# Optimization experiments

Hardware: AMD Instinct MI355X
Metric: run time of the kernel (lower is better)

Reference implementation:

```python
import jax, jax.numpy as jnp
import numpy as np

# AllOrNothing: spike threshold (x > 0) with straight-through gradient.
@jax.custom_vjp
def aon(x):
    return (x > 0).astype(x.dtype)

def _aon_fwd(x):
    return aon(x), None

def _aon_bwd(_, g):
    return (g,)

aon.defvjp(_aon_fwd, _aon_bwd)

T, B = 1000, 128
N_IN, N_H, N_PC, N_HD, N_IC = 3, 256, 256, 12, 268


def setup_inputs() -> dict:
    key = jax.random.key(0)
    ks = jax.random.split(key, 13)
    f32 = jnp.float32
    inp = {
        "x": jax.random.normal(ks[0], (T, B, N_IN), f32),
        "initial_conds": jax.random.normal(ks[1], (B, N_IC), f32),
        # RecurrentSNUCell params
        "iw": jax.random.normal(ks[2], (N_IN, N_H), f32) / np.sqrt(N_IN),  # kaiming-ish
        "l": jax.random.normal(ks[3], (N_H,), f32) / np.sqrt(N_H),          # trunc-normal-ish
        "b": jnp.zeros((N_H,), f32),
        # Linear layers, stored as [in, out] for x @ W + b
        "state_embed_w": jax.random.normal(ks[4], (N_IC, N_H), f32) / np.sqrt(128.0),
        "state_embed_b": jnp.zeros((N_H,), f32),
        "cell_embed_w": jax.random.normal(ks[5], (N_IC, N_H), f32) / np.sqrt(128.0),
        "cell_embed_b": jnp.zeros((N_H,), f32),
        "pc_w": jax.random.normal(ks[6], (N_H, N_PC), f32) / np.sqrt(256.0),
        "pc_b": jnp.zeros((N_PC,), f32),
        "hd_w": jax.random.normal(ks[7], (N_H, N_HD), f32) / np.sqrt(12.0),
        "hd_b": jnp.zeros((N_HD,), f32),
    }
    return inp


def reference(x, initial_conds, iw, l, b,
              state_embed_w, state_embed_b, cell_embed_w, cell_embed_b,
              pc_w, pc_b, hd_w, hd_b):
    # init = cat(initial_conds); here a single [B, 268] tensor
    h0 = jax.nn.sigmoid(initial_conds @ state_embed_w + state_embed_b)  # y_0 [B,H]
    c0 = jax.nn.sigmoid(initial_conds @ cell_embed_w + cell_embed_b)    # s_0 [B,H]

    def step(carry, x_t):
        h, c = carry  # (y_t, s_t)
        # RecurrentSNUCell: s = relu(x@iw + y + l*s*(1-y)); y = aon(s + b)
        s = jax.nn.relu(x_t @ iw + h + l * c * (1.0 - h))
        y = aon(s + b)
        # dropout in eval mode -> identity
        pc = y @ pc_w + pc_b
        hd = y @ hd_w + hd_b
        return (y, s), (hd, pc, y, y, s)

    _, (logits_hd, logits_pc, bottleneck_acts, rnn_states, cell_states) = \
        jax.lax.scan(step, (h0, c0), x)
    return (logits_hd, logits_pc, bottleneck_acts, rnn_states, cell_states)
```

## Files before the change

### kernel.cpp

```cpp
#include <hip/hip_runtime.h>
#include <hip/hip_bf16.h>
#include <math.h>

#define T_STEPS 1000
#define BATCH   128
#define NH      256
#define NIC     268
#define NHD     12

#define SZ_HD (T_STEPS * BATCH * NHD)
#define SZ_PC (T_STEPS * BATCH * NH)
#define OFF_HD 0
#define OFF_PC (SZ_HD)
#define OFF_BA (OFF_PC + SZ_PC)
#define OFF_RS (OFF_BA + SZ_PC)
#define OFF_CS (OFF_RS + SZ_PC)

typedef __attribute__((ext_vector_type(8))) short short8;
typedef __attribute__((ext_vector_type(4))) float float4v;

static __device__ __forceinline__ unsigned short f32_to_bf16_bits(float v) {
    __hip_bfloat16 h = __float2bfloat16(v);
    return *reinterpret_cast<unsigned short*>(&h);
}

__global__ __launch_bounds__(64) void recurrence_kernel(
    const float* __restrict__ x,
    const float* __restrict__ ic,
    const float* __restrict__ iw,
    const float* __restrict__ l,
    const float* __restrict__ bvec,
    const float* __restrict__ sew,
    const float* __restrict__ seb,
    const float* __restrict__ cew,
    const float* __restrict__ ceb,
    float* __restrict__ out)
{
    const int blk = blockIdx.x;
    const int b   = blk >> 2;
    const int h   = ((blk & 3) << 6) | (threadIdx.x & 63);

    double ah = (double)seb[h];
    double ac = (double)ceb[h];
    const float* icrow = ic + (size_t)b * NIC;
    for (int k = 0; k < NIC; ++k) {
        const double v = (double)icrow[k];
        ah += v * (double)sew[(size_t)k * NH + h];
        ac += v * (double)cew[(size_t)k * NH + h];
    }
    double y = 1.0 / (1.0 + exp(-ah));
    double c = 1.0 / (1.0 + exp(-ac));

    const double lv = (double)l[h];
    const double bv = (double)bvec[h];
    const double w0 = (double)iw[h];
    const double w1 = (double)iw[NH + h];
    const double w2 = (double)iw[2 * NH + h];

    const float* xp = x + (size_t)b * 3;
    float* __restrict__ out_ba = out + OFF_BA;
    float* __restrict__ out_rs = out + OFF_RS;
    float* __restrict__ out_cs = out + OFF_CS;

    const size_t obase = (size_t)b * NH + h;

    float bufA[30], bufB[30];

    auto pre_load = [&](float* bf, int tb) {
#pragma unroll
        for (int u = 0; u < 10; ++u) {
            const float* p = xp + (size_t)(tb + u) * (BATCH * 3);
            bf[u * 3 + 0] = p[0];
            bf[u * 3 + 1] = p[1];
            bf[u * 3 + 2] = p[2];
        }
    };

    auto comp10 = [&](const float* bf, int tb) {
#pragma unroll
        for (int u = 0; u < 10; ++u) {
            const double x0 = (double)bf[u * 3 + 0];
            const double x1 = (double)bf[u * 3 + 1];
            const double x2 = (double)bf[u * 3 + 2];
            const double dot = x0 * w0 + x1 * w1 + x2 * w2;
            const double pre = (dot + y) + (lv * c) * (1.0 - y);
            const double s   = fmax(pre, 0.0);
            const double yn  = (s + bv > 0.0) ? 1.0 : 0.0;
            const size_t o = obase + (size_t)(tb + u) * (BATCH * NH);
            out_ba[o] = (float)yn;
            out_rs[o] = (float)yn;
            out_cs[o] = (float)s;
            y = yn;
            c = s;
        }
    };

    pre_load(bufA, 0);
    for (int tb = 0; tb < T_STEPS; tb += 20) {
        if (tb + 10 < T_STEPS) pre_load(bufB, tb + 10);
        comp10(bufA, tb);
        if (tb + 20 < T_STEPS) pre_load(bufA, tb + 20);
        comp10(bufB, tb + 10);
    }
}

__global__ __launch_bounds__(256) void wcvt_kernel(
    const float* __restrict__ pc_w,
    const float* __restrict__ hd_w,
    unsigned short* __restrict__ bt)
{
    const int n = blockIdx.x;
    const int k = threadIdx.x;
    float v;
    if (n < NH)            v = pc_w[(size_t)k * NH + n];
    else if (n < NH + NHD) v = hd_w[(size_t)k * NHD + (n - NH)];
    else                   v = 0.0f;
    bt[(size_t)n * NH + k] = f32_to_bf16_bits(v);
}

template <bool USE_WS>
__global__ __launch_bounds__(256, 2) void gemm_kernel(
    const float* __restrict__ out_base,
    const unsigned short* __restrict__ bt,
    const float* __restrict__ pc_w,
    const float* __restrict__ hd_w,
    const float* __restrict__ pc_b,
    const float* __restrict__ hd_b,
    float* __restrict__ out)
{
    __shared__ unsigned short Alds[64][264];
    const int tid  = threadIdx.x;
    const int wave = tid >> 6;
    const int lane = tid & 63;
    const int r0   = blockIdx.x * 64;

    const float* __restrict__ Y = out_base + OFF_BA;

    for (int i = 0; i < 16; ++i) {
        const int idx = i * 256 + tid;
        const int row = idx >> 6;
        const int kc  = (idx & 63) * 4;
        const float4v v = *reinterpret_cast<const float4v*>(
            Y + (size_t)(r0 + row) * NH + kc);
        const unsigned int u0 = (unsigned int)f32_to_bf16_bits(v.x) |
                                ((unsigned int)f32_to_bf16_bits(v.y) << 16);
        const unsigned int u1 = (unsigned int)f32_to_bf16_bits(v.z) |
                                ((unsigned int)f32_to_bf16_bits(v.w) << 16);
        const unsigned long long u = (unsigned long long)u0 |
                                     ((unsigned long long)u1 << 32);
        *reinterpret_cast<unsigned long long*>(&Alds[row][kc]) = u;
    }
    __syncthreads();

    const int m = lane & 15;
    const int q = lane >> 4;

    float4v acc[17];
    for (int t = 0; t < 16; ++t) {
        const float bb = pc_b[t * 16 + m];
        acc[t] = (float4v){bb, bb, bb, bb};
    }
    {
        const float bb = (m < NHD) ? hd_b[m] : 0.0f;
        acc[16] = (float4v){bb, bb, bb, bb};
    }

    for (int ks = 0; ks < 8; ++ks) {
        short8 bfr[17];
        if constexpr (USE_WS) {
#pragma unroll
            for (int t = 0; t < 17; ++t)
                bfr[t] = *reinterpret_cast<const short8*>(
                    bt + ((size_t)(t * 16 + m) * NH + ks * 32 + q * 8));
        } else {
#pragma unroll
            for (int t = 0; t < 17; ++t) {
                const int n = t * 16 + m;
#pragma unroll
                for (int j = 0; j < 8; ++j) {
                    const int kk = ks * 32 + q * 8 + j;
                    float v;
                    if (n < NH)            v = pc_w[(size_t)kk * NH + n];
                    else if (n < NH + NHD) v = hd_w[(size_t)kk * NHD + (n - NH)];
                    else                   v = 0.0f;
                    bfr[t][j] = (short)f32_to_bf16_bits(v);
                }
            }
        }
        const short8 a = *reinterpret_cast<const short8*>(
            &Alds[wave * 16 + m][ks * 32 + q * 8]);
#pragma unroll
        for (int t = 0; t < 17; ++t)
            acc[t] = __builtin_amdgcn_mfma_f32_16x16x32_bf16(a, bfr[t], acc[t], 0, 0, 0);
    }

    float* __restrict__ out_pc = out + OFF_PC;
    float* __restrict__ out_hd = out + OFF_HD;
    const int rowb = r0 + wave * 16 + q * 4;
#pragma unroll
    for (int t = 0; t < 16; ++t) {
        const int col = t * 16 + m;
#pragma unroll
        for (int r = 0; r < 4; ++r)
            out_pc[(size_t)(rowb + r) * NH + col] = acc[t][r];
    }
    if (m < NHD) {
#pragma unroll
        for (int r = 0; r < 4; ++r)
            out_hd[(size_t)(rowb + r) * NHD + m] = acc[16][r];
    }
}

extern "C" void kernel_launch(void* const* d_in, const int* in_sizes, int n_in,
                              void* d_out, int out_size, void* d_ws, size_t ws_size,
                              hipStream_t stream) {
    const float* x    = (const float*)d_in[0];
    const float* ic   = (const float*)d_in[1];
    const float* iw   = (const float*)d_in[2];
    const float* l    = (const float*)d_in[3];
    const float* bb   = (const float*)d_in[4];
    const float* sew  = (const float*)d_in[5];
    const float* seb  = (const float*)d_in[6];
    const float* cew  = (const float*)d_in[7];
    const float* ceb  = (const float*)d_in[8];
    const float* pc_w = (const float*)d_in[9];
    const float* pc_b = (const float*)d_in[10];
    const float* hd_w = (const float*)d_in[11];
    const float* hd_b = (const float*)d_in[12];
    float* out = (float*)d_out;

    const bool use_ws = ws_size >= (size_t)(272 * 256 * 2);
    unsigned short* bt = (unsigned short*)d_ws;

    if (use_ws) {
        wcvt_kernel<<<272, 256, 0, stream>>>(pc_w, hd_w, bt);
    }
    recurrence_kernel<<<512, 64, 0, stream>>>(x, ic, iw, l, bb,
                                              sew, seb, cew, ceb, out);
    if (use_ws) {
        gemm_kernel<true><<<2000, 256, 0, stream>>>(out, bt, pc_w, hd_w,
                                                    pc_b, hd_b, out);
    } else {
        gemm_kernel<false><<<2000, 256, 0, stream>>>(out, nullptr, pc_w, hd_w,
                                                     pc_b, hd_b, out);
    }
}
```

Measured before the change: 807.2 us.

## Pack spike outputs as ballot bitmasks and expand them in the GEMM kernel

The recurrence kernel no longer writes the two float spike tensors. Each wave ballots its spikes into a 64-bit mask stored in workspace, and the GEMM kernel expands those masks into the bf16 A tile and writes the bottleneck and rnn-state outputs with vectorized stores. This takes two scattered fp32 stores per step off the latency-bound serial recurrence and replaces the GEMM's fp32 reread of activations with a small bitmask read. The B-fragment loads are also regrouped into batches of four to lower register pressure. The cost is an extra workspace requirement and a ballot plus one lane-0 store per step.

```diff
diff --git a/kernel.cpp b/kernel.cpp
--- a/kernel.cpp
+++ b/kernel.cpp
@@ -24,6 +24,7 @@
     return *reinterpret_cast<unsigned short*>(&h);
 }
 
+template <bool BITS>
 __global__ __launch_bounds__(64) void recurrence_kernel(
     const float* __restrict__ x,
     const float* __restrict__ ic,
@@ -34,11 +35,14 @@
     const float* __restrict__ seb,
     const float* __restrict__ cew,
     const float* __restrict__ ceb,
-    float* __restrict__ out)
+    float* __restrict__ out,
+    unsigned long long* __restrict__ bits)
 {
-    const int blk = blockIdx.x;
-    const int b   = blk >> 2;
-    const int h   = ((blk & 3) << 6) | (threadIdx.x & 63);
+    const int blk  = blockIdx.x;
+    const int b    = blk >> 2;
+    const int hq   = blk & 3;
+    const int lane = threadIdx.x & 63;
+    const int h    = (hq << 6) | lane;
 
     double ah = (double)seb[h];
     double ac = (double)ceb[h];
@@ -85,12 +89,19 @@
             const double dot = x0 * w0 + x1 * w1 + x2 * w2;
             const double pre = (dot + y) + (lv * c) * (1.0 - y);
             const double s   = fmax(pre, 0.0);
-            const double yn  = (s + bv > 0.0) ? 1.0 : 0.0;
+            const bool spike = (s + bv > 0.0);
             const size_t o = obase + (size_t)(tb + u) * (BATCH * NH);
-            out_ba[o] = (float)yn;
-            out_rs[o] = (float)yn;
             out_cs[o] = (float)s;
-            y = yn;
+            if constexpr (BITS) {
+                const unsigned long long mk = __ballot((int)spike);
+                if (lane == 0)
+                    bits[((size_t)(tb + u) * BATCH + b) * 4 + hq] = mk;
+            } else {
+                const float yf = spike ? 1.0f : 0.0f;
+                out_ba[o] = yf;
+                out_rs[o] = yf;
+            }
+            y = spike ? 1.0 : 0.0;
             c = s;
         }
     };
@@ -116,6 +127,102 @@
     else if (n < NH + NHD) v = hd_w[(size_t)k * NHD + (n - NH)];
     else                   v = 0.0f;
     bt[(size_t)n * NH + k] = f32_to_bf16_bits(v);
+}
+
+__global__ __launch_bounds__(256, 2) void gemm_bits_kernel(
+    const unsigned long long* __restrict__ bits,
+    const unsigned short* __restrict__ bt,
+    const float* __restrict__ pc_b,
+    const float* __restrict__ hd_b,
+    float* __restrict__ out)
+{
+    __shared__ unsigned short Alds[64][264];
+    const int tid  = threadIdx.x;
+    const int wave = tid >> 6;
+    const int lane = tid & 63;
+    const int r0   = blockIdx.x * 64;
+
+    {
+        const int rA = tid & 63, wA = tid >> 6;
+        const unsigned long long mA = bits[(size_t)(r0 + rA) * 4 + wA];
+#pragma unroll
+        for (int j8 = 0; j8 < 8; ++j8) {
+            short8 v;
+#pragma unroll
+            for (int j = 0; j < 8; ++j)
+                v[j] = (short)(((mA >> (j8 * 8 + j)) & 1ull) ? 0x3F80 : 0);
+            *reinterpret_cast<short8*>(&Alds[rA][wA * 64 + j8 * 8]) = v;
+        }
+    }
+
+    {
+        const int rB = tid >> 2, wB = tid & 3;
+        const unsigned long long mB = bits[(size_t)(r0 + rB) * 4 + wB];
+        float* __restrict__ out_ba = out + OFF_BA;
+        float* __restrict__ out_rs = out + OFF_RS;
+        const size_t base = (size_t)(r0 + rB) * NH + wB * 64;
+#pragma unroll
+        for (int j4 = 0; j4 < 16; ++j4) {
+            float4v v;
+#pragma unroll
+            for (int j = 0; j < 4; ++j)
+                v[j] = ((mB >> (j4 * 4 + j)) & 1ull) ? 1.0f : 0.0f;
+            *reinterpret_cast<float4v*>(&out_ba[base + j4 * 4]) = v;
+            *reinterpret_cast<float4v*>(&out_rs[base + j4 * 4]) = v;
+        }
+    }
+    __syncthreads();
+
+    const int m = lane & 15;
+    const int q = lane >> 4;
+
+    float4v acc[17];
+    for (int t = 0; t < 16; ++t) {
+        const float bb = pc_b[t * 16 + m];
+        acc[t] = (float4v){bb, bb, bb, bb};
+    }
+    {
+        const float bb = (m < NHD) ? hd_b[m] : 0.0f;
+        acc[16] = (float4v){bb, bb, bb, bb};
+    }
+
+    for (int ks = 0; ks < 8; ++ks) {
+        const short8 a = *reinterpret_cast<const short8*>(
+            &Alds[wave * 16 + m][ks * 32 + q * 8]);
+#pragma unroll
+        for (int g = 0; g < 4; ++g) {
+            short8 bfr[4];
+#pragma unroll
+            for (int t = 0; t < 4; ++t)
+                bfr[t] = *reinterpret_cast<const short8*>(
+                    bt + ((size_t)((g * 4 + t) * 16 + m) * NH + ks * 32 + q * 8));
+#pragma unroll
+            for (int t = 0; t < 4; ++t)
+                acc[g * 4 + t] = __builtin_amdgcn_mfma_f32_16x16x32_bf16(
+                    a, bfr[t], acc[g * 4 + t], 0, 0, 0);
+        }
+        {
+            const short8 bh = *reinterpret_cast<const short8*>(
+                bt + ((size_t)(16 * 16 + m) * NH + ks * 32 + q * 8));
+            acc[16] = __builtin_amdgcn_mfma_f32_16x16x32_bf16(a, bh, acc[16], 0, 0, 0);
+        }
+    }
+
+    float* __restrict__ out_pc = out + OFF_PC;
+    float* __restrict__ out_hd = out + OFF_HD;
+    const int rowb = r0 + wave * 16 + q * 4;
+#pragma unroll
+    for (int t = 0; t < 16; ++t) {
+        const int col = t * 16 + m;
+#pragma unroll
+        for (int r = 0; r < 4; ++r)
+            out_pc[(size_t)(rowb + r) * NH + col] = acc[t][r];
+    }
+    if (m < NHD) {
+#pragma unroll
+        for (int r = 0; r < 4; ++r)
+            out_hd[(size_t)(rowb + r) * NHD + m] = acc[16][r];
+    }
 }
 
 template <bool USE_WS>
@@ -166,32 +273,53 @@
     }
 
     for (int ks = 0; ks < 8; ++ks) {
-        short8 bfr[17];
-        if constexpr (USE_WS) {
-#pragma unroll
-            for (int t = 0; t < 17; ++t)
-                bfr[t] = *reinterpret_cast<const short8*>(
-                    bt + ((size_t)(t * 16 + m) * NH + ks * 32 + q * 8));
-        } else {
-#pragma unroll
-            for (int t = 0; t < 17; ++t) {
-                const int n = t * 16 + m;
+        const short8 a = *reinterpret_cast<const short8*>(
+            &Alds[wave * 16 + m][ks * 32 + q * 8]);
+#pragma unroll
+        for (int g = 0; g < 4; ++g) {
+            short8 bfr[4];
+#pragma unroll
+            for (int t = 0; t < 4; ++t) {
+                const int tt = g * 4 + t;
+                if constexpr (USE_WS) {
+                    bfr[t] = *reinterpret_cast<const short8*>(
+                        bt + ((size_t)(tt * 16 + m) * NH + ks * 32 + q * 8));
+                } else {
+                    const int n = tt * 16 + m;
+#pragma unroll
+                    for (int j = 0; j < 8; ++j) {
+                        const int kk = ks * 32 + q * 8 + j;
+                        float v;
+                        if (n < NH)            v = pc_w[(size_t)kk * NH + n];
+                        else if (n < NH + NHD) v = hd_w[(size_t)kk * NHD + (n - NH)];
+                        else                   v = 0.0f;
+                        bfr[t][j] = (short)f32_to_bf16_bits(v);
+                    }
+                }
+            }
+#pragma unroll
+            for (int t = 0; t < 4; ++t)
+                acc[g * 4 + t] = __builtin_amdgcn_mfma_f32_16x16x32_bf16(
+                    a, bfr[t], acc[g * 4 + t], 0, 0, 0);
+        }
+        {
+            short8 bh;
+            if constexpr (USE_WS) {
+                bh = *reinterpret_cast<const short8*>(
+                    bt + ((size_t)(256 + m) * NH + ks * 32 + q * 8));
+            } else {
 #pragma unroll
                 for (int j = 0; j < 8; ++j) {
                     const int kk = ks * 32 + q * 8 + j;
+                    const int n = 256 + m;
                     float v;
-                    if (n < NH)            v = pc_w[(size_t)kk * NH + n];
-                    else if (n < NH + NHD) v = hd_w[(size_t)kk * NHD + (n - NH)];
-                    else                   v = 0.0f;
-                    bfr[t][j] = (short)f32_to_bf16_bits(v);
+                    if (n < NH + NHD) v = hd_w[(size_t)kk * NHD + (n - NH)];
+                    else              v = 0.0f;
+                    bh[j] = (short)f32_to_bf16_bits(v);
                 }
             }
-        }
-        const short8 a = *reinterpret_cast<const short8*>(
-            &Alds[wave * 16 + m][ks * 32 + q * 8]);
-#pragma unroll
-        for (int t = 0; t < 17; ++t)
-            acc[t] = __builtin_amdgcn_mfma_f32_16x16x32_bf16(a, bfr[t], acc[t], 0, 0, 0);
+            acc[16] = __builtin_amdgcn_mfma_f32_16x16x32_bf16(a, bh, acc[16], 0, 0, 0);
+        }
     }
 
     float* __restrict__ out_pc = out + OFF_PC;
@@ -229,18 +357,29 @@
     const float* hd_b = (const float*)d_in[12];
     float* out = (float*)d_out;
 
-    const bool use_ws = ws_size >= (size_t)(272 * 256 * 2);
+    const size_t BT_BYTES   = (size_t)272 * 256 * 2;
+    const size_t BITS_BYTES = (size_t)T_STEPS * BATCH * 4 * 8;
     unsigned short* bt = (unsigned short*)d_ws;
-
-    if (use_ws) {
+    unsigned long long* bits =
+        (unsigned long long*)((char*)d_ws + BT_BYTES);
+
+    if (ws_size >= BT_BYTES + BITS_BYTES) {
         wcvt_kernel<<<272, 256, 0, stream>>>(pc_w, hd_w, bt);
-    }
-    recurrence_kernel<<<512, 64, 0, stream>>>(x, ic, iw, l, bb,
-                                              sew, seb, cew, ceb, out);
-    if (use_ws) {
+        recurrence_kernel<true><<<512, 64, 0, stream>>>(x, ic, iw, l, bb,
+                                                        sew, seb, cew, ceb,
+                                                        out, bits);
+        gemm_bits_kernel<<<2000, 256, 0, stream>>>(bits, bt, pc_b, hd_b, out);
+    } else if (ws_size >= BT_BYTES) {
+        wcvt_kernel<<<272, 256, 0, stream>>>(pc_w, hd_w, bt);
+        recurrence_kernel<false><<<512, 64, 0, stream>>>(x, ic, iw, l, bb,
+                                                         sew, seb, cew, ceb,
+                                                         out, nullptr);
         gemm_kernel<true><<<2000, 256, 0, stream>>>(out, bt, pc_w, hd_w,
                                                     pc_b, hd_b, out);
     } else {
+        recurrence_kernel<false><<<512, 64, 0, stream>>>(x, ic, iw, l, bb,
+                                                         sew, seb, cew, ceb,
+                                                         out, nullptr);
         gemm_kernel<false><<<2000, 256, 0, stream>>>(out, nullptr, pc_w, hd_w,
                                                      pc_b, hd_b, out);
     }
```

After: 914.9 us. 1.13x slower.
